# Kernel tuning notes

Measured on AMD Instinct MI355X. Metric: run time of the kernel, lower is better.

## Reference

```python
import jax, jax.numpy as jnp
import numpy as np

N_NODES = 50000
N_EDGES = 600000
IN_DIM = 128
HID = 128
N_CLASSES = 40
N_GRAPHS = 128


def setup_inputs() -> dict:
    key = jax.random.key(0)
    ks = jax.random.split(key, 12)
    x = jax.random.normal(ks[0], (N_NODES, IN_DIM), dtype=jnp.float32)
    edge_index = jax.random.randint(ks[1], (2, N_EDGES), 0, N_NODES, dtype=jnp.int64)
    batch = jnp.sort(jax.random.randint(ks[2], (N_NODES,), 0, N_GRAPHS, dtype=jnp.int64))
    dims = [IN_DIM, HID, HID, N_CLASSES]
    params = {}
    for l in range(3):
        d_in, d_out = dims[l], dims[l + 1]
        s = 1.0 / np.sqrt(d_in)
        params[f"Wl{l}"] = jax.random.uniform(ks[3 + 3 * l], (d_out, d_in), jnp.float32, -s, s)
        params[f"bl{l}"] = jax.random.uniform(ks[4 + 3 * l], (d_out,), jnp.float32, -s, s)
        params[f"Wr{l}"] = jax.random.uniform(ks[5 + 3 * l], (d_out, d_in), jnp.float32, -s, s)
    return {"x": x, "edge_index": edge_index, "batch": batch, **params}


def _sage_layer(h, src, dst, Wl, bl, Wr):
    # message: relu(x_j) (edge_attr is None -> zero), mean-aggregate at dst
    m = jnp.maximum(h[src], 0.0)                       # [E, d]
    agg = jax.ops.segment_sum(m, dst, num_segments=N_NODES)
    cnt = jax.ops.segment_sum(jnp.ones((m.shape[0],), h.dtype), dst, num_segments=N_NODES)
    agg = agg / jnp.maximum(cnt, 1.0)[:, None]
    # lin_l(agg) + lin_r(x)
    return agg @ Wl.T + bl + h @ Wr.T


def reference(x, edge_index, batch, Wl0, bl0, Wr0, Wl1, bl1, Wr1, Wl2, bl2, Wr2):
    src, dst = edge_index[0], edge_index[1]
    Ws = [(Wl0, bl0, Wr0), (Wl1, bl1, Wr1), (Wl2, bl2, Wr2)]
    h = x
    for l, (Wl, bl, Wr) in enumerate(Ws):
        # dropout is identity in eval mode
        h = _sage_layer(h, src, dst, Wl, bl, Wr)
        if l != len(Ws) - 1:
            h = jnp.maximum(h, 0.0)
    # global mean pool over graphs
    gsum = jax.ops.segment_sum(h, batch, num_segments=N_GRAPHS)
    gcnt = jax.ops.segment_sum(jnp.ones((h.shape[0],), h.dtype), batch, num_segments=N_GRAPHS)
    g = gsum / jnp.maximum(gcnt, 1.0)[:, None]
    return h, g
```

## Files before the change

### kernel.cpp

```cpp
#include <hip/hip_runtime.h>
#include <hip/hip_bf16.h>


#define NODES 50000
#define K_DIM 128
#define N_GRAPHS 128

typedef __attribute__((ext_vector_type(8))) short short8;
typedef __attribute__((ext_vector_type(4))) short short4v;
typedef __attribute__((ext_vector_type(4))) float f32x4;

__device__ inline short f2bf(float f) {
    unsigned u = __builtin_bit_cast(unsigned, f);
    u += 0x7FFFu + ((u >> 16) & 1u);
    return (short)(u >> 16);
}
__device__ inline float bf2f(short h) {
    unsigned u = ((unsigned)(unsigned short)h) << 16;
    return __builtin_bit_cast(float, u);
}
__device__ inline float blo(unsigned u) { return __builtin_bit_cast(float, u << 16); }
__device__ inline float bhi(unsigned u) { return __builtin_bit_cast(float, u & 0xFFFF0000u); }
__device__ inline unsigned hilo_pack(float f) {
    short h = f2bf(f);
    short l = f2bf(f - bf2f(h));
    return ((unsigned)(unsigned short)h) | (((unsigned)(unsigned short)l) << 16);
}

__global__ void init_kernel(const float* __restrict__ w0, const float* __restrict__ w1,
                            const float* __restrict__ w2, const float* __restrict__ w3,
                            const float* __restrict__ w4, const float* __restrict__ w5,
                            short* __restrict__ whi, short* __restrict__ wlo,
                            int* __restrict__ deg, const int* __restrict__ batch,
                            int* __restrict__ gstart,
                            const float* __restrict__ x, short* __restrict__ xb,
                            short* __restrict__ xhi, short* __restrict__ xlo, int N) {
    int idx = blockIdx.x * 256 + threadIdx.x;
    if (idx < N * (K_DIM / 4)) {
        float4 v = reinterpret_cast<const float4*>(x)[idx];
        unsigned px = hilo_pack(v.x), py = hilo_pack(v.y);
        unsigned pz = hilo_pack(v.z), pw = hilo_pack(v.w);
        short4v b, hh, ll;
        b[0] = f2bf(fmaxf(v.x, 0.f)); hh[0] = (short)(px & 0xFFFFu); ll[0] = (short)(px >> 16);
        b[1] = f2bf(fmaxf(v.y, 0.f)); hh[1] = (short)(py & 0xFFFFu); ll[1] = (short)(py >> 16);
        b[2] = f2bf(fmaxf(v.z, 0.f)); hh[2] = (short)(pz & 0xFFFFu); ll[2] = (short)(pz >> 16);
        b[3] = f2bf(fmaxf(v.w, 0.f)); hh[3] = (short)(pw & 0xFFFFu); ll[3] = (short)(pw >> 16);
        *reinterpret_cast<short4v*>(&xb [idx * 4]) = b;
        *reinterpret_cast<short4v*>(&xhi[idx * 4]) = hh;
        *reinterpret_cast<short4v*>(&xlo[idx * 4]) = ll;
    }
    if (idx < N) deg[idx] = 0;
    const int TOT = 4 * 16384 + 96 * 128;
    if (idx < TOT) {
        float v;
        if (idx < 65536) {
            int m = idx >> 14, e = idx & 16383;
            const float* W = (m == 0) ? w0 : (m == 1) ? w1 : (m == 2) ? w2 : w3;
            v = W[e];
        } else {
            int i2 = idx - 65536;
            int row = i2 >> 7, col = i2 & 127;
            if (row < 40)      v = w4[row * 128 + col];
            else if (row < 80) v = w5[(row - 40) * 128 + col];
            else               v = 0.f;
        }
        unsigned p = hilo_pack(v);
        whi[idx] = (short)(p & 0xFFFFu);
        wlo[idx] = (short)(p >> 16);
    }
    if (idx <= N_GRAPHS) {
        int g = idx;
        int lo = 0, hi = N;
        while (lo < hi) {
            int mid = (lo + hi) >> 1;
            if (batch[mid] < g) lo = mid + 1; else hi = mid;
        }
        gstart[g] = lo;
    }
}

__global__ void deg_kernel(const int* __restrict__ dst, int* __restrict__ deg, int E) {
    int e = blockIdx.x * blockDim.x + threadIdx.x;
    if (e < E) atomicAdd(&deg[dst[e]], 1);
}

__global__ void scan_p1(const int* __restrict__ deg, int* __restrict__ bsum, int N) {
    int i = blockIdx.x * 256 + threadIdx.x;
    int v = (i < N) ? deg[i] : 0;
    #pragma unroll
    for (int off = 32; off > 0; off >>= 1) v += __shfl_down(v, off, 64);
    __shared__ int ws[4];
    int lane = threadIdx.x & 63, wv = threadIdx.x >> 6;
    if (lane == 0) ws[wv] = v;
    __syncthreads();
    if (threadIdx.x == 0) bsum[blockIdx.x] = ws[0] + ws[1] + ws[2] + ws[3];
}

__global__ void scan_p23(const int* __restrict__ deg, const int* __restrict__ bsum,
                         int* __restrict__ rowptr, int* __restrict__ fillpos,
                         int N, int NB) {
    const int tid = threadIdx.x, lane = tid & 63, wv = tid >> 6;
    __shared__ int ws[4];
    __shared__ int sboff[256];
    {
        int v = (tid < NB) ? bsum[tid] : 0;
        int incl = v;
        #pragma unroll
        for (int off = 1; off < 64; off <<= 1) {
            int t = __shfl_up(incl, off, 64);
            if (lane >= off) incl += t;
        }
        if (lane == 63) ws[wv] = incl;
        __syncthreads();
        int add = 0;
        for (int k = 0; k < wv; ++k) add += ws[k];
        sboff[tid] = incl + add - v;
        __syncthreads();
    }
    const int boff = sboff[blockIdx.x];
    int i = blockIdx.x * 256 + tid;
    int v = (i < N) ? deg[i] : 0;
    int incl = v;
    #pragma unroll
    for (int off = 1; off < 64; off <<= 1) {
        int t = __shfl_up(incl, off, 64);
        if (lane >= off) incl += t;
    }
    __shared__ int ws2[4];
    if (lane == 63) ws2[wv] = incl;
    __syncthreads();
    int add = 0;
    for (int k = 0; k < wv; ++k) add += ws2[k];
    int excl = boff + incl + add - v;
    if (i < N) { rowptr[i] = excl; fillpos[i] = excl; }
    if (i == N) rowptr[N] = excl;
}

__global__ void fill_kernel(const int* __restrict__ src, const int* __restrict__ dst,
                            int* __restrict__ fillpos, int* __restrict__ csr_src, int E) {
    int e = blockIdx.x * blockDim.x + threadIdx.x;
    if (e < E) {
        int p = atomicAdd(&fillpos[dst[e]], 1);
        csr_src[p] = src[e];
    }
}

__global__ void agg_bf16(const unsigned short* __restrict__ hb,
                         const int* __restrict__ rowptr,
                         const int* __restrict__ csr_src,
                         short* __restrict__ aggb, int N) {
    int w = (blockIdx.x * blockDim.x + threadIdx.x) >> 6;
    if (w >= N) return;
    int lane = threadIdx.x & 63;
    int half = lane >> 5, l32 = lane & 31;
    int s = rowptr[w], e = rowptr[w + 1];
    float4 acc = make_float4(0.f, 0.f, 0.f, 0.f);
    int i = s + half;
    for (; i + 6 < e; i += 8) {
        int s0 = csr_src[i], s1 = csr_src[i + 2], s2 = csr_src[i + 4], s3 = csr_src[i + 6];
        uint2 v0 = reinterpret_cast<const uint2*>(hb + (size_t)s0 * K_DIM)[l32];
        uint2 v1 = reinterpret_cast<const uint2*>(hb + (size_t)s1 * K_DIM)[l32];
        uint2 v2 = reinterpret_cast<const uint2*>(hb + (size_t)s2 * K_DIM)[l32];
        uint2 v3 = reinterpret_cast<const uint2*>(hb + (size_t)s3 * K_DIM)[l32];
        acc.x += (blo(v0.x) + blo(v1.x)) + (blo(v2.x) + blo(v3.x));
        acc.y += (bhi(v0.x) + bhi(v1.x)) + (bhi(v2.x) + bhi(v3.x));
        acc.z += (blo(v0.y) + blo(v1.y)) + (blo(v2.y) + blo(v3.y));
        acc.w += (bhi(v0.y) + bhi(v1.y)) + (bhi(v2.y) + bhi(v3.y));
    }
    for (; i < e; i += 2) {
        int s0 = csr_src[i];
        uint2 v0 = reinterpret_cast<const uint2*>(hb + (size_t)s0 * K_DIM)[l32];
        acc.x += blo(v0.x); acc.y += bhi(v0.x);
        acc.z += blo(v0.y); acc.w += bhi(v0.y);
    }
    acc.x += __shfl_xor(acc.x, 32, 64);
    acc.y += __shfl_xor(acc.y, 32, 64);
    acc.z += __shfl_xor(acc.z, 32, 64);
    acc.w += __shfl_xor(acc.w, 32, 64);
    if (half == 0) {
        float inv = 1.0f / fmaxf((float)(e - s), 1.0f);
        short4v b;
        b[0] = f2bf(acc.x * inv);
        b[1] = f2bf(acc.y * inv);
        b[2] = f2bf(acc.z * inv);
        b[3] = f2bf(acc.w * inv);
        *reinterpret_cast<short4v*>(&aggb[(size_t)w * K_DIM + l32 * 4]) = b;
    }
}

__global__ __launch_bounds__(256) void sage_mfma(
        const short* __restrict__ Ab_in,
        const short* __restrict__ Hhi_in, const short* __restrict__ Hlo_in,
        const short* __restrict__ Bhl, const short* __restrict__ Bll,
        const short* __restrict__ Bhr, const short* __restrict__ Blr,
        const float* __restrict__ bl,
        short* __restrict__ outHi, short* __restrict__ outLo, int N) {
    constexpr int BM = 64;
    constexpr int LSTR = 40;
    const int tid = threadIdx.x;
    const int lane = tid & 63;
    const int wave = tid >> 6;
    const int l15 = lane & 15;
    const int quad = lane >> 4;
    const int m0 = blockIdx.x * BM;
    const int srow = tid >> 2, sc8 = tid & 3;

    __shared__ __align__(16) short Ahi[BM * LSTR];
    __shared__ __align__(16) short Alo[BM * LSTR];

    f32x4 acc[4][2];
    #pragma unroll
    for (int i = 0; i < 4; ++i)
        #pragma unroll
        for (int j = 0; j < 2; ++j) acc[i][j] = (f32x4){0.f, 0.f, 0.f, 0.f};

    const short8 zero8 = (short8){0, 0, 0, 0, 0, 0, 0, 0};
    const int sm = m0 + srow;

    for (int k0 = 0; k0 < K_DIM; k0 += 32) {
        __syncthreads();
        {
            short8 v = zero8;
            if (sm < N) v = *reinterpret_cast<const short8*>(Ab_in + (size_t)sm * K_DIM + k0 + sc8 * 8);
            *reinterpret_cast<short8*>(&Ahi[srow * LSTR + sc8 * 8]) = v;
        }
        short8 bh[2], bo[2];
        #pragma unroll
        for (int nt = 0; nt < 2; ++nt) {
            int n = wave * 32 + nt * 16 + l15;
            bh[nt] = *reinterpret_cast<const short8*>(Bhl + (size_t)n * K_DIM + k0 + quad * 8);
            bo[nt] = *reinterpret_cast<const short8*>(Bll + (size_t)n * K_DIM + k0 + quad * 8);
        }
        __syncthreads();
        #pragma unroll
        for (int mt = 0; mt < 4; ++mt) {
            int row = mt * 16 + l15;
            short8 ab = *reinterpret_cast<const short8*>(&Ahi[row * LSTR + quad * 8]);
            #pragma unroll
            for (int nt = 0; nt < 2; ++nt) {
                acc[mt][nt] = __builtin_amdgcn_mfma_f32_16x16x32_bf16(ab, bh[nt], acc[mt][nt], 0, 0, 0);
                acc[mt][nt] = __builtin_amdgcn_mfma_f32_16x16x32_bf16(ab, bo[nt], acc[mt][nt], 0, 0, 0);
            }
        }
    }

    for (int k0 = 0; k0 < K_DIM; k0 += 32) {
        __syncthreads();
        {
            short8 vh = zero8, vl = zero8;
            if (sm < N) {
                vh = *reinterpret_cast<const short8*>(Hhi_in + (size_t)sm * K_DIM + k0 + sc8 * 8);
                vl = *reinterpret_cast<const short8*>(Hlo_in + (size_t)sm * K_DIM + k0 + sc8 * 8);
            }
            *reinterpret_cast<short8*>(&Ahi[srow * LSTR + sc8 * 8]) = vh;
            *reinterpret_cast<short8*>(&Alo[srow * LSTR + sc8 * 8]) = vl;
        }
        short8 bh[2], bo[2];
        #pragma unroll
        for (int nt = 0; nt < 2; ++nt) {
            int n = wave * 32 + nt * 16 + l15;
            bh[nt] = *reinterpret_cast<const short8*>(Bhr + (size_t)n * K_DIM + k0 + quad * 8);
            bo[nt] = *reinterpret_cast<const short8*>(Blr + (size_t)n * K_DIM + k0 + quad * 8);
        }
        __syncthreads();
        #pragma unroll
        for (int mt = 0; mt < 4; ++mt) {
            int row = mt * 16 + l15;
            short8 ah = *reinterpret_cast<const short8*>(&Ahi[row * LSTR + quad * 8]);
            short8 ao = *reinterpret_cast<const short8*>(&Alo[row * LSTR + quad * 8]);
            #pragma unroll
            for (int nt = 0; nt < 2; ++nt) {
                acc[mt][nt] = __builtin_amdgcn_mfma_f32_16x16x32_bf16(ah, bh[nt], acc[mt][nt], 0, 0, 0);
                acc[mt][nt] = __builtin_amdgcn_mfma_f32_16x16x32_bf16(ah, bo[nt], acc[mt][nt], 0, 0, 0);
                acc[mt][nt] = __builtin_amdgcn_mfma_f32_16x16x32_bf16(ao, bh[nt], acc[mt][nt], 0, 0, 0);
            }
        }
    }

    #pragma unroll
    for (int mt = 0; mt < 4; ++mt) {
        #pragma unroll
        for (int nt = 0; nt < 2; ++nt) {
            int col = wave * 32 + nt * 16 + l15;
            float b = bl[col];
            #pragma unroll
            for (int reg = 0; reg < 4; ++reg) {
                int row = m0 + mt * 16 + quad * 4 + reg;
                if (row < N) {
                    float v = fmaxf(acc[mt][nt][reg] + b, 0.f);
                    unsigned p = hilo_pack(v);
                    outHi[(size_t)row * K_DIM + col] = (short)(p & 0xFFFFu);
                    outLo[(size_t)row * K_DIM + col] = (short)(p >> 16);
                }
            }
        }
    }
}

__global__ __launch_bounds__(256) void gemm80(
        const short* __restrict__ Xhi, const short* __restrict__ Xlo,
        const short* __restrict__ Bh, const short* __restrict__ Bv,
        const float* __restrict__ b2,
        short* __restrict__ ylb, float* __restrict__ yr40, int N) {
    constexpr int BM = 64;
    constexpr int LSTR = 40;
    const int tid = threadIdx.x;
    const int lane = tid & 63;
    const int wave = tid >> 6;
    const int wm = wave & 1;
    const int wn = wave >> 1;
    const int l15 = lane & 15;
    const int quad = lane >> 4;
    const int m0 = blockIdx.x * BM;
    const int srow = tid >> 2, sc8 = tid & 3;

    __shared__ __align__(16) short Ahi[BM * LSTR];
    __shared__ __align__(16) short Alo[BM * LSTR];

    f32x4 acc[2][3];
    #pragma unroll
    for (int i = 0; i < 2; ++i)
        #pragma unroll
        for (int j = 0; j < 3; ++j) acc[i][j] = (f32x4){0.f, 0.f, 0.f, 0.f};

    const short8 zero8 = (short8){0, 0, 0, 0, 0, 0, 0, 0};
    const int sm = m0 + srow;

    for (int k0 = 0; k0 < K_DIM; k0 += 32) {
        __syncthreads();
        {
            short8 vh = zero8, vl = zero8;
            if (sm < N) {
                vh = *reinterpret_cast<const short8*>(Xhi + (size_t)sm * K_DIM + k0 + sc8 * 8);
                vl = *reinterpret_cast<const short8*>(Xlo + (size_t)sm * K_DIM + k0 + sc8 * 8);
            }
            *reinterpret_cast<short8*>(&Ahi[srow * LSTR + sc8 * 8]) = vh;
            *reinterpret_cast<short8*>(&Alo[srow * LSTR + sc8 * 8]) = vl;
        }
        short8 bh[3], bo[3];
        #pragma unroll
        for (int nt = 0; nt < 3; ++nt) {
            int n = wn * 48 + nt * 16 + l15;
            bh[nt] = *reinterpret_cast<const short8*>(Bh + (size_t)n * K_DIM + k0 + quad * 8);
            bo[nt] = *reinterpret_cast<const short8*>(Bv + (size_t)n * K_DIM + k0 + quad * 8);
        }
        __syncthreads();
        #pragma unroll
        for (int mt = 0; mt < 2; ++mt) {
            int row = wm * 32 + mt * 16 + l15;
            short8 ah = *reinterpret_cast<const short8*>(&Ahi[row * LSTR + quad * 8]);
            short8 ao = *reinterpret_cast<const short8*>(&Alo[row * LSTR + quad * 8]);
            #pragma unroll
            for (int nt = 0; nt < 3; ++nt) {
                acc[mt][nt] = __builtin_amdgcn_mfma_f32_16x16x32_bf16(ah, bh[nt], acc[mt][nt], 0, 0, 0);
                acc[mt][nt] = __builtin_amdgcn_mfma_f32_16x16x32_bf16(ah, bo[nt], acc[mt][nt], 0, 0, 0);
                acc[mt][nt] = __builtin_amdgcn_mfma_f32_16x16x32_bf16(ao, bh[nt], acc[mt][nt], 0, 0, 0);
            }
        }
    }

    #pragma unroll
    for (int mt = 0; mt < 2; ++mt) {
        #pragma unroll
        for (int nt = 0; nt < 3; ++nt) {
            int col = wn * 48 + nt * 16 + l15;
            #pragma unroll
            for (int reg = 0; reg < 4; ++reg) {
                int row = m0 + wm * 32 + mt * 16 + quad * 4 + reg;
                if (row < N) {
                    float v = acc[mt][nt][reg];
                    if (col < 40) {
                        ylb[(size_t)row * 40 + col] = f2bf(v);
                    } else if (col < 80) {
                        yr40[(size_t)row * 40 + (col - 40)] = v + b2[col - 40];
                    }
                }
            }
        }
    }
}

__global__ void agg40_kernel(const unsigned short* __restrict__ ylb,
                             const float* __restrict__ yr40,
                             const int* __restrict__ rowptr, const int* __restrict__ csr_src,
                             float* __restrict__ out, int N) {
    int w = (blockIdx.x * blockDim.x + threadIdx.x) >> 6;
    if (w >= N) return;
    int lane = threadIdx.x & 63;
    int s = rowptr[w], e = rowptr[w + 1];
    if (lane >= 40) return;
    float acc = 0.f;
    int i = s;
    for (; i + 3 < e; i += 4) {
        int s0 = csr_src[i], s1 = csr_src[i + 1], s2 = csr_src[i + 2], s3 = csr_src[i + 3];
        float v0 = bf2f((short)ylb[(size_t)s0 * 40 + lane]);
        float v1 = bf2f((short)ylb[(size_t)s1 * 40 + lane]);
        float v2 = bf2f((short)ylb[(size_t)s2 * 40 + lane]);
        float v3 = bf2f((short)ylb[(size_t)s3 * 40 + lane]);
        acc += (v0 + v1) + (v2 + v3);
    }
    for (; i < e; ++i) acc += bf2f((short)ylb[(size_t)csr_src[i] * 40 + lane]);
    float inv = 1.0f / fmaxf((float)(e - s), 1.0f);
    out[(size_t)w * 40 + lane] = acc * inv + yr40[(size_t)w * 40 + lane];
}

__global__ __launch_bounds__(320) void pool_kernel(const float* __restrict__ h,
                                                   const int* __restrict__ gstart,
                                                   float* __restrict__ g_out) {
    int g = blockIdx.x;
    int tid = threadIdx.x;
    int c = tid % 40, r = tid / 40;
    int s = gstart[g], e = gstart[g + 1];
    float acc = 0.f;
    for (int n = s + r; n < e; n += 8)
        acc += h[(size_t)n * 40 + c];
    __shared__ float sh[8][40];
    sh[r][c] = acc;
    __syncthreads();
    if (r == 0) {
        float sum = 0.f;
        #pragma unroll
        for (int i = 0; i < 8; ++i) sum += sh[i][c];
        g_out[g * 40 + c] = sum / fmaxf((float)(e - s), 1.0f);
    }
}

extern "C" void kernel_launch(void* const* d_in, const int* in_sizes, int n_in,
                              void* d_out, int out_size, void* d_ws, size_t ws_size,
                              hipStream_t stream) {
    const float* x    = (const float*)d_in[0];
    const int*   ei   = (const int*)d_in[1];
    const int*   batch= (const int*)d_in[2];
    const float* Wl0  = (const float*)d_in[3];
    const float* bl0  = (const float*)d_in[4];
    const float* Wr0  = (const float*)d_in[5];
    const float* Wl1  = (const float*)d_in[6];
    const float* bl1  = (const float*)d_in[7];
    const float* Wr1  = (const float*)d_in[8];
    const float* Wl2  = (const float*)d_in[9];
    const float* bl2  = (const float*)d_in[10];
    const float* Wr2  = (const float*)d_in[11];

    const int N = in_sizes[0] / K_DIM;
    const int E = in_sizes[1] / 2;
    const int* src = ei;
    const int* dst = ei + E;

    float* out = (float*)d_out;
    float* gsum = out + (size_t)N * 40;

    char* w = (char*)d_ws;
    auto alloc = [&](size_t bytes) {
        char* p = w;
        w += (bytes + 255) & ~(size_t)255;
        return p;
    };
    const size_t PL = (size_t)N * K_DIM * 2;
    short* aggb  = (short*)alloc(PL);
    short* xb    = (short*)alloc(PL);
    short* xhi   = (short*)alloc(PL);
    short* xlo   = (short*)alloc(PL);
    short* h1hi  = (short*)alloc(PL);
    short* h1lo  = (short*)alloc(PL);
    short* h2hi  = (short*)alloc(PL);
    short* h2lo  = (short*)alloc(PL);
    short* ylb   = (short*)alloc((size_t)N * 40 * 2);
    float* yr40  = (float*)alloc((size_t)N * 40 * 4);
    int*   rowptr= (int*)alloc((size_t)(N + 1) * 4);
    int*   deg   = (int*)alloc((size_t)N * 4);
    int*   fillp = (int*)alloc((size_t)N * 4);
    int*   csr   = (int*)alloc((size_t)E * 4);
    int*   bsum  = (int*)alloc(256 * 4);
    int*   gstart= (int*)alloc((size_t)(N_GRAPHS + 1) * 4);
    short* whi   = (short*)alloc(77824 * 2);
    short* wlo   = (short*)alloc(77824 * 2);

    const int NB = (N + 255) / 256;
    const int initGrid = (N * (K_DIM / 4) + 255) / 256;

    init_kernel<<<initGrid, 256, 0, stream>>>(Wl0, Wr0, Wl1, Wr1, Wl2, Wr2,
                                              whi, wlo, deg, batch, gstart,
                                              x, xb, xhi, xlo, N);
    deg_kernel<<<(E + 255) / 256, 256, 0, stream>>>(dst, deg, E);
    scan_p1<<<NB, 256, 0, stream>>>(deg, bsum, N);
    scan_p23<<<NB, 256, 0, stream>>>(deg, bsum, rowptr, fillp, N, NB);
    fill_kernel<<<(E + 255) / 256, 256, 0, stream>>>(src, dst, fillp, csr, E);

    short* hWl0 = whi;          short* lWl0 = wlo;
    short* hWr0 = whi + 16384;  short* lWr0 = wlo + 16384;
    short* hWl1 = whi + 32768;  short* lWl1 = wlo + 32768;
    short* hWr1 = whi + 49152;  short* lWr1 = wlo + 49152;
    short* hW2  = whi + 65536;  short* lW2  = wlo + 65536;

    const int aggGrid  = (N * 64 + 255) / 256;
    const int gemmGrid = (N + 63) / 64;

    agg_bf16<<<aggGrid, 256, 0, stream>>>((const unsigned short*)xb, rowptr, csr, aggb, N);
    sage_mfma<<<gemmGrid, 256, 0, stream>>>(
        aggb, xhi, xlo, hWl0, lWl0, hWr0, lWr0, bl0, h1hi, h1lo, N);
    agg_bf16<<<aggGrid, 256, 0, stream>>>((const unsigned short*)h1hi, rowptr, csr, aggb, N);
    sage_mfma<<<gemmGrid, 256, 0, stream>>>(
        aggb, h1hi, h1lo, hWl1, lWl1, hWr1, lWr1, bl1, h2hi, h2lo, N);
    gemm80<<<gemmGrid, 256, 0, stream>>>(h2hi, h2lo, hW2, lW2, bl2, ylb, yr40, N);
    agg40_kernel<<<aggGrid, 256, 0, stream>>>((const unsigned short*)ylb, yr40, rowptr, csr, out, N);

    pool_kernel<<<N_GRAPHS, 320, 0, stream>>>(out, gstart, gsum);
}
```

Baseline: 336.1 us.

## Fuse CSR build into cooperative kernel, merge GEMM K-loops, fuse pooling into aggregation

Five preprocessing kernels (init, degree count, two scan passes, CSR fill) become one cooperative kernel with grid-wide syncs. The scan now recomputes each block's prefix by summing all earlier degrees, which costs quadratic reads. The two K-loops in sage_mfma are merged into one pass that stages three A tiles in shared memory. The final aggregation also does global mean pooling through atomics into gsum, replacing the separate pool kernel. These cut launch count and GEMM barriers but add atomic contention and a nondeterministic float summation order for the pooled output.

```diff
diff --git a/kernel.cpp b/kernel.cpp
--- a/kernel.cpp
+++ b/kernel.cpp
@@ -1,5 +1,8 @@
 #include <hip/hip_runtime.h>
 #include <hip/hip_bf16.h>
+#include <hip/hip_cooperative_groups.h>
+
+namespace cg = cooperative_groups;
 
 
 #define NODES 50000
@@ -27,16 +30,54 @@
     return ((unsigned)(unsigned short)h) | (((unsigned)(unsigned short)l) << 16);
 }
 
-__global__ void init_kernel(const float* __restrict__ w0, const float* __restrict__ w1,
-                            const float* __restrict__ w2, const float* __restrict__ w3,
-                            const float* __restrict__ w4, const float* __restrict__ w5,
-                            short* __restrict__ whi, short* __restrict__ wlo,
-                            int* __restrict__ deg, const int* __restrict__ batch,
-                            int* __restrict__ gstart,
-                            const float* __restrict__ x, short* __restrict__ xb,
-                            short* __restrict__ xhi, short* __restrict__ xlo, int N) {
-    int idx = blockIdx.x * 256 + threadIdx.x;
-    if (idx < N * (K_DIM / 4)) {
+__global__ __launch_bounds__(256, 2) void frontend(
+        const float* __restrict__ w0, const float* __restrict__ w1,
+        const float* __restrict__ w2, const float* __restrict__ w3,
+        const float* __restrict__ w4, const float* __restrict__ w5,
+        short* __restrict__ whi, short* __restrict__ wlo,
+        const float* __restrict__ x, short* __restrict__ xb,
+        short* __restrict__ xhi, short* __restrict__ xlo,
+        const int* __restrict__ batch, int* __restrict__ gstart,
+        const int* __restrict__ src, const int* __restrict__ dst,
+        int* __restrict__ deg, int* __restrict__ rowptr,
+        int* __restrict__ fillpos, int* __restrict__ csr,
+        float* __restrict__ gsum,
+        int N, int E, int NB) {
+    cg::grid_group grid = cg::this_grid();
+    const int gs  = gridDim.x * blockDim.x;
+    const int id0 = blockIdx.x * blockDim.x + threadIdx.x;
+
+    for (int i = id0; i < N; i += gs) deg[i] = 0;
+    for (int i = id0; i < N_GRAPHS * 40; i += gs) gsum[i] = 0.f;
+    for (int i = id0; i < 77824; i += gs) {
+        float v;
+        if (i < 65536) {
+            int m = i >> 14, e2 = i & 16383;
+            const float* W = (m == 0) ? w0 : (m == 1) ? w1 : (m == 2) ? w2 : w3;
+            v = W[e2];
+        } else {
+            int i2 = i - 65536;
+            int row = i2 >> 7, col = i2 & 127;
+            if (row < 40)      v = w4[row * 128 + col];
+            else if (row < 80) v = w5[(row - 40) * 128 + col];
+            else               v = 0.f;
+        }
+        unsigned p = hilo_pack(v);
+        whi[i] = (short)(p & 0xFFFFu);
+        wlo[i] = (short)(p >> 16);
+    }
+    for (int g = id0; g <= N_GRAPHS; g += gs) {
+        int lo = 0, hi2 = N;
+        while (lo < hi2) {
+            int mid = (lo + hi2) >> 1;
+            if (batch[mid] < g) lo = mid + 1; else hi2 = mid;
+        }
+        gstart[g] = lo;
+    }
+    grid.sync();
+
+    for (int e = id0; e < E; e += gs) atomicAdd(&deg[dst[e]], 1);
+    for (int idx = id0; idx < N * (K_DIM / 4); idx += gs) {
         float4 v = reinterpret_cast<const float4*>(x)[idx];
         unsigned px = hilo_pack(v.x), py = hilo_pack(v.y);
         unsigned pz = hilo_pack(v.z), pw = hilo_pack(v.w);
@@ -49,99 +90,43 @@
         *reinterpret_cast<short4v*>(&xhi[idx * 4]) = hh;
         *reinterpret_cast<short4v*>(&xlo[idx * 4]) = ll;
     }
-    if (idx < N) deg[idx] = 0;
-    const int TOT = 4 * 16384 + 96 * 128;
-    if (idx < TOT) {
-        float v;
-        if (idx < 65536) {
-            int m = idx >> 14, e = idx & 16383;
-            const float* W = (m == 0) ? w0 : (m == 1) ? w1 : (m == 2) ? w2 : w3;
-            v = W[e];
-        } else {
-            int i2 = idx - 65536;
-            int row = i2 >> 7, col = i2 & 127;
-            if (row < 40)      v = w4[row * 128 + col];
-            else if (row < 80) v = w5[(row - 40) * 128 + col];
-            else               v = 0.f;
-        }
-        unsigned p = hilo_pack(v);
-        whi[idx] = (short)(p & 0xFFFFu);
-        wlo[idx] = (short)(p >> 16);
-    }
-    if (idx <= N_GRAPHS) {
-        int g = idx;
-        int lo = 0, hi = N;
-        while (lo < hi) {
-            int mid = (lo + hi) >> 1;
-            if (batch[mid] < g) lo = mid + 1; else hi = mid;
-        }
-        gstart[g] = lo;
-    }
-}
-
-__global__ void deg_kernel(const int* __restrict__ dst, int* __restrict__ deg, int E) {
-    int e = blockIdx.x * blockDim.x + threadIdx.x;
-    if (e < E) atomicAdd(&deg[dst[e]], 1);
-}
-
-__global__ void scan_p1(const int* __restrict__ deg, int* __restrict__ bsum, int N) {
-    int i = blockIdx.x * 256 + threadIdx.x;
-    int v = (i < N) ? deg[i] : 0;
-    #pragma unroll
-    for (int off = 32; off > 0; off >>= 1) v += __shfl_down(v, off, 64);
+    grid.sync();
+
     __shared__ int ws[4];
-    int lane = threadIdx.x & 63, wv = threadIdx.x >> 6;
-    if (lane == 0) ws[wv] = v;
-    __syncthreads();
-    if (threadIdx.x == 0) bsum[blockIdx.x] = ws[0] + ws[1] + ws[2] + ws[3];
-}
-
-__global__ void scan_p23(const int* __restrict__ deg, const int* __restrict__ bsum,
-                         int* __restrict__ rowptr, int* __restrict__ fillpos,
-                         int N, int NB) {
-    const int tid = threadIdx.x, lane = tid & 63, wv = tid >> 6;
-    __shared__ int ws[4];
-    __shared__ int sboff[256];
-    {
-        int v = (tid < NB) ? bsum[tid] : 0;
+    __shared__ int ws2[4];
+    for (int c = blockIdx.x; c < NB; c += gridDim.x) {
+        const int tid = threadIdx.x, lane = tid & 63, wv = tid >> 6;
+        const int start = c * 256;
+        int part = 0;
+        for (int j = tid; j < start; j += 256) part += deg[j];
+        #pragma unroll
+        for (int off = 32; off > 0; off >>= 1) part += __shfl_down(part, off, 64);
+        if (lane == 0) ws[wv] = part;
+        __syncthreads();
+        const int base = ws[0] + ws[1] + ws[2] + ws[3];
+        int i = start + tid;
+        int v = (i < N) ? deg[i] : 0;
         int incl = v;
         #pragma unroll
         for (int off = 1; off < 64; off <<= 1) {
             int t = __shfl_up(incl, off, 64);
             if (lane >= off) incl += t;
         }
-        if (lane == 63) ws[wv] = incl;
+        if (lane == 63) ws2[wv] = incl;
         __syncthreads();
         int add = 0;
-        for (int k = 0; k < wv; ++k) add += ws[k];
-        sboff[tid] = incl + add - v;
-        __syncthreads();
-    }
-    const int boff = sboff[blockIdx.x];
-    int i = blockIdx.x * 256 + tid;
-    int v = (i < N) ? deg[i] : 0;
-    int incl = v;
-    #pragma unroll
-    for (int off = 1; off < 64; off <<= 1) {
-        int t = __shfl_up(incl, off, 64);
-        if (lane >= off) incl += t;
-    }
-    __shared__ int ws2[4];
-    if (lane == 63) ws2[wv] = incl;
-    __syncthreads();
-    int add = 0;
-    for (int k = 0; k < wv; ++k) add += ws2[k];
-    int excl = boff + incl + add - v;
-    if (i < N) { rowptr[i] = excl; fillpos[i] = excl; }
-    if (i == N) rowptr[N] = excl;
-}
-
-__global__ void fill_kernel(const int* __restrict__ src, const int* __restrict__ dst,
-                            int* __restrict__ fillpos, int* __restrict__ csr_src, int E) {
-    int e = blockIdx.x * blockDim.x + threadIdx.x;
-    if (e < E) {
+        for (int k = 0; k < wv; ++k) add += ws2[k];
+        const int tot = incl + add;
+        const int excl = base + tot - v;
+        if (i < N) { rowptr[i] = excl; fillpos[i] = excl; }
+        if (c == NB - 1 && tid == 255) rowptr[N] = base + tot;
+        __syncthreads();
+    }
+    grid.sync();
+
+    for (int e = id0; e < E; e += gs) {
         int p = atomicAdd(&fillpos[dst[e]], 1);
-        csr_src[p] = src[e];
+        csr[p] = src[e];
     }
 }
 
@@ -205,6 +190,7 @@
     const int m0 = blockIdx.x * BM;
     const int srow = tid >> 2, sc8 = tid & 3;
 
+    __shared__ __align__(16) short Ab [BM * LSTR];
     __shared__ __align__(16) short Ahi[BM * LSTR];
     __shared__ __align__(16) short Alo[BM * LSTR];
 
@@ -220,59 +206,40 @@
     for (int k0 = 0; k0 < K_DIM; k0 += 32) {
         __syncthreads();
         {
-            short8 v = zero8;
-            if (sm < N) v = *reinterpret_cast<const short8*>(Ab_in + (size_t)sm * K_DIM + k0 + sc8 * 8);
-            *reinterpret_cast<short8*>(&Ahi[srow * LSTR + sc8 * 8]) = v;
-        }
-        short8 bh[2], bo[2];
+            short8 va = zero8, vh = zero8, vl = zero8;
+            if (sm < N) {
+                va = *reinterpret_cast<const short8*>(Ab_in  + (size_t)sm * K_DIM + k0 + sc8 * 8);
+                vh = *reinterpret_cast<const short8*>(Hhi_in + (size_t)sm * K_DIM + k0 + sc8 * 8);
+                vl = *reinterpret_cast<const short8*>(Hlo_in + (size_t)sm * K_DIM + k0 + sc8 * 8);
+            }
+            *reinterpret_cast<short8*>(&Ab [srow * LSTR + sc8 * 8]) = va;
+            *reinterpret_cast<short8*>(&Ahi[srow * LSTR + sc8 * 8]) = vh;
+            *reinterpret_cast<short8*>(&Alo[srow * LSTR + sc8 * 8]) = vl;
+        }
+        short8 bhl_[2], bll_[2], bhr_[2], blr_[2];
         #pragma unroll
         for (int nt = 0; nt < 2; ++nt) {
             int n = wave * 32 + nt * 16 + l15;
-            bh[nt] = *reinterpret_cast<const short8*>(Bhl + (size_t)n * K_DIM + k0 + quad * 8);
-            bo[nt] = *reinterpret_cast<const short8*>(Bll + (size_t)n * K_DIM + k0 + quad * 8);
+            size_t off = (size_t)n * K_DIM + k0 + quad * 8;
+            bhl_[nt] = *reinterpret_cast<const short8*>(Bhl + off);
+            bll_[nt] = *reinterpret_cast<const short8*>(Bll + off);
+            bhr_[nt] = *reinterpret_cast<const short8*>(Bhr + off);
+            blr_[nt] = *reinterpret_cast<const short8*>(Blr + off);
         }
         __syncthreads();
         #pragma unroll
         for (int mt = 0; mt < 4; ++mt) {
             int row = mt * 16 + l15;
-            short8 ab = *reinterpret_cast<const short8*>(&Ahi[row * LSTR + quad * 8]);
-            #pragma unroll
-            for (int nt = 0; nt < 2; ++nt) {
-                acc[mt][nt] = __builtin_amdgcn_mfma_f32_16x16x32_bf16(ab, bh[nt], acc[mt][nt], 0, 0, 0);
-                acc[mt][nt] = __builtin_amdgcn_mfma_f32_16x16x32_bf16(ab, bo[nt], acc[mt][nt], 0, 0, 0);
-            }
-        }
-    }
-
-    for (int k0 = 0; k0 < K_DIM; k0 += 32) {
-        __syncthreads();
-        {
-            short8 vh = zero8, vl = zero8;
-            if (sm < N) {
-                vh = *reinterpret_cast<const short8*>(Hhi_in + (size_t)sm * K_DIM + k0 + sc8 * 8);
-                vl = *reinterpret_cast<const short8*>(Hlo_in + (size_t)sm * K_DIM + k0 + sc8 * 8);
-            }
-            *reinterpret_cast<short8*>(&Ahi[srow * LSTR + sc8 * 8]) = vh;
-            *reinterpret_cast<short8*>(&Alo[srow * LSTR + sc8 * 8]) = vl;
-        }
-        short8 bh[2], bo[2];
-        #pragma unroll
-        for (int nt = 0; nt < 2; ++nt) {
-            int n = wave * 32 + nt * 16 + l15;
-            bh[nt] = *reinterpret_cast<const short8*>(Bhr + (size_t)n * K_DIM + k0 + quad * 8);
-            bo[nt] = *reinterpret_cast<const short8*>(Blr + (size_t)n * K_DIM + k0 + quad * 8);
-        }
-        __syncthreads();
-        #pragma unroll
-        for (int mt = 0; mt < 4; ++mt) {
-            int row = mt * 16 + l15;
+            short8 ab = *reinterpret_cast<const short8*>(&Ab [row * LSTR + quad * 8]);
             short8 ah = *reinterpret_cast<const short8*>(&Ahi[row * LSTR + quad * 8]);
             short8 ao = *reinterpret_cast<const short8*>(&Alo[row * LSTR + quad * 8]);
             #pragma unroll
             for (int nt = 0; nt < 2; ++nt) {
-                acc[mt][nt] = __builtin_amdgcn_mfma_f32_16x16x32_bf16(ah, bh[nt], acc[mt][nt], 0, 0, 0);
-                acc[mt][nt] = __builtin_amdgcn_mfma_f32_16x16x32_bf16(ah, bo[nt], acc[mt][nt], 0, 0, 0);
-                acc[mt][nt] = __builtin_amdgcn_mfma_f32_16x16x32_bf16(ao, bh[nt], acc[mt][nt], 0, 0, 0);
+                acc[mt][nt] = __builtin_amdgcn_mfma_f32_16x16x32_bf16(ab, bhl_[nt], acc[mt][nt], 0, 0, 0);
+                acc[mt][nt] = __builtin_amdgcn_mfma_f32_16x16x32_bf16(ab, bll_[nt], acc[mt][nt], 0, 0, 0);
+                acc[mt][nt] = __builtin_amdgcn_mfma_f32_16x16x32_bf16(ah, bhr_[nt], acc[mt][nt], 0, 0, 0);
+                acc[mt][nt] = __builtin_amdgcn_mfma_f32_16x16x32_bf16(ah, blr_[nt], acc[mt][nt], 0, 0, 0);
+                acc[mt][nt] = __builtin_amdgcn_mfma_f32_16x16x32_bf16(ao, bhr_[nt], acc[mt][nt], 0, 0, 0);
             }
         }
     }
@@ -380,48 +347,65 @@
     }
 }
 
-__global__ void agg40_kernel(const unsigned short* __restrict__ ylb,
-                             const float* __restrict__ yr40,
-                             const int* __restrict__ rowptr, const int* __restrict__ csr_src,
-                             float* __restrict__ out, int N) {
-    int w = (blockIdx.x * blockDim.x + threadIdx.x) >> 6;
-    if (w >= N) return;
-    int lane = threadIdx.x & 63;
-    int s = rowptr[w], e = rowptr[w + 1];
-    if (lane >= 40) return;
-    float acc = 0.f;
-    int i = s;
-    for (; i + 3 < e; i += 4) {
-        int s0 = csr_src[i], s1 = csr_src[i + 1], s2 = csr_src[i + 2], s3 = csr_src[i + 3];
-        float v0 = bf2f((short)ylb[(size_t)s0 * 40 + lane]);
-        float v1 = bf2f((short)ylb[(size_t)s1 * 40 + lane]);
-        float v2 = bf2f((short)ylb[(size_t)s2 * 40 + lane]);
-        float v3 = bf2f((short)ylb[(size_t)s3 * 40 + lane]);
-        acc += (v0 + v1) + (v2 + v3);
-    }
-    for (; i < e; ++i) acc += bf2f((short)ylb[(size_t)csr_src[i] * 40 + lane]);
-    float inv = 1.0f / fmaxf((float)(e - s), 1.0f);
-    out[(size_t)w * 40 + lane] = acc * inv + yr40[(size_t)w * 40 + lane];
-}
-
-__global__ __launch_bounds__(320) void pool_kernel(const float* __restrict__ h,
-                                                   const int* __restrict__ gstart,
-                                                   float* __restrict__ g_out) {
-    int g = blockIdx.x;
-    int tid = threadIdx.x;
-    int c = tid % 40, r = tid / 40;
-    int s = gstart[g], e = gstart[g + 1];
-    float acc = 0.f;
-    for (int n = s + r; n < e; n += 8)
-        acc += h[(size_t)n * 40 + c];
-    __shared__ float sh[8][40];
-    sh[r][c] = acc;
+__global__ __launch_bounds__(256) void agg40_pool(
+        const unsigned short* __restrict__ ylb, const float* __restrict__ yr40,
+        const int* __restrict__ rowptr, const int* __restrict__ csr_src,
+        const int* __restrict__ batch, const int* __restrict__ gstart,
+        float* __restrict__ out, float* __restrict__ gsum, int N) {
+    const int w = (blockIdx.x * blockDim.x + threadIdx.x) >> 6;
+    const int lane = threadIdx.x & 63;
+    const int wv = threadIdx.x >> 6;
+    __shared__ float sh[4][40];
+    __shared__ int sg[4];
+    __shared__ float sinv[4];
+
+    float val = 0.f;
+    const bool valid = (w < N) && (lane < 40);
+    if (valid) {
+        int s = rowptr[w], e = rowptr[w + 1];
+        float acc = 0.f;
+        int i = s;
+        for (; i + 3 < e; i += 4) {
+            int s0 = csr_src[i], s1 = csr_src[i + 1], s2 = csr_src[i + 2], s3 = csr_src[i + 3];
+            float v0 = bf2f((short)ylb[(size_t)s0 * 40 + lane]);
+            float v1 = bf2f((short)ylb[(size_t)s1 * 40 + lane]);
+            float v2 = bf2f((short)ylb[(size_t)s2 * 40 + lane]);
+            float v3 = bf2f((short)ylb[(size_t)s3 * 40 + lane]);
+            acc += (v0 + v1) + (v2 + v3);
+        }
+        for (; i < e; ++i) acc += bf2f((short)ylb[(size_t)csr_src[i] * 40 + lane]);
+        float inv = 1.0f / fmaxf((float)(e - s), 1.0f);
+        val = acc * inv + yr40[(size_t)w * 40 + lane];
+        out[(size_t)w * 40 + lane] = val;
+        sh[wv][lane] = val;
+    }
+    if (lane == 0) {
+        if (w < N) {
+            int g = batch[w];
+            sg[wv] = g;
+            sinv[wv] = 1.0f / fmaxf((float)(gstart[g + 1] - gstart[g]), 1.0f);
+        } else {
+            sg[wv] = -1;
+        }
+    }
     __syncthreads();
-    if (r == 0) {
-        float sum = 0.f;
-        #pragma unroll
-        for (int i = 0; i < 8; ++i) sum += sh[i][c];
-        g_out[g * 40 + c] = sum / fmaxf((float)(e - s), 1.0f);
+    if (wv == 0 && lane < 40) {
+        int cur = -1;
+        float accum = 0.f;
+        #pragma unroll
+        for (int k = 0; k < 4; ++k) {
+            int gk = sg[k];
+            if (gk < 0) continue;
+            float c = sh[k][lane] * sinv[k];
+            if (gk == cur) {
+                accum += c;
+            } else {
+                if (cur >= 0) atomicAdd(&gsum[cur * 40 + lane], accum);
+                cur = gk;
+                accum = c;
+            }
+        }
+        if (cur >= 0) atomicAdd(&gsum[cur * 40 + lane], accum);
     }
 }
 
@@ -470,21 +454,23 @@
     int*   deg   = (int*)alloc((size_t)N * 4);
     int*   fillp = (int*)alloc((size_t)N * 4);
     int*   csr   = (int*)alloc((size_t)E * 4);
-    int*   bsum  = (int*)alloc(256 * 4);
     int*   gstart= (int*)alloc((size_t)(N_GRAPHS + 1) * 4);
     short* whi   = (short*)alloc(77824 * 2);
     short* wlo   = (short*)alloc(77824 * 2);
 
-    const int NB = (N + 255) / 256;
-    const int initGrid = (N * (K_DIM / 4) + 255) / 256;
-
-    init_kernel<<<initGrid, 256, 0, stream>>>(Wl0, Wr0, Wl1, Wr1, Wl2, Wr2,
-                                              whi, wlo, deg, batch, gstart,
-                                              x, xb, xhi, xlo, N);
-    deg_kernel<<<(E + 255) / 256, 256, 0, stream>>>(dst, deg, E);
-    scan_p1<<<NB, 256, 0, stream>>>(deg, bsum, N);
-    scan_p23<<<NB, 256, 0, stream>>>(deg, bsum, rowptr, fillp, N, NB);
-    fill_kernel<<<(E + 255) / 256, 256, 0, stream>>>(src, dst, fillp, csr, E);
+    int Nv = N, Ev = E, NBv = (N + 255) / 256;
+
+    void* kargs[] = {
+        (void*)&Wl0, (void*)&Wr0, (void*)&Wl1, (void*)&Wr1, (void*)&Wl2, (void*)&Wr2,
+        (void*)&whi, (void*)&wlo,
+        (void*)&x, (void*)&xb, (void*)&xhi, (void*)&xlo,
+        (void*)&batch, (void*)&gstart,
+        (void*)&src, (void*)&dst,
+        (void*)&deg, (void*)&rowptr, (void*)&fillp, (void*)&csr,
+        (void*)&gsum,
+        (void*)&Nv, (void*)&Ev, (void*)&NBv };
+    hipLaunchCooperativeKernel((const void*)frontend, dim3(512), dim3(256),
+                               kargs, 0, stream);
 
     short* hWl0 = whi;          short* lWl0 = wlo;
     short* hWr0 = whi + 16384;  short* lWr0 = wlo + 16384;
@@ -502,7 +488,6 @@
     sage_mfma<<<gemmGrid, 256, 0, stream>>>(
         aggb, h1hi, h1lo, hWl1, lWl1, hWr1, lWr1, bl1, h2hi, h2lo, N);
     gemm80<<<gemmGrid, 256, 0, stream>>>(h2hi, h2lo, hW2, lW2, bl2, ylb, yr40, N);
-    agg40_kernel<<<aggGrid, 256, 0, stream>>>((const unsigned short*)ylb, yr40, rowptr, csr, out, N);
-
-    pool_kernel<<<N_GRAPHS, 320, 0, stream>>>(out, gstart, gsum);
-}
+    agg40_pool<<<aggGrid, 256, 0, stream>>>((const unsigned short*)ylb, yr40,
+                                            rowptr, csr, batch, gstart, out, gsum, N);
+}
```

Measured after the change: 554.6 us. +65.0%, slower.
